# Kernel tuning notes

Hardware: AMD Instinct MI355X
Metric: run time of the kernel (lower is better)

The kernel has to match this reference:

```python
import jax, jax.numpy as jnp
import numpy as np

B, T, C = 2, 2048, 1024
H = 16
HD = C // H  # 64


def setup_inputs() -> dict:
    key = jax.random.key(0)
    ks = jax.random.split(key, 6)
    s_in = 1.0 / np.sqrt(C)
    s_pr = 1.0 / np.sqrt(H * HD)
    x = jax.random.normal(ks[0], (B, T, C), dtype=jnp.float32)
    Wq = jax.random.uniform(ks[1], (H, C, HD), jnp.float32, -s_in, s_in)
    Wk = jax.random.uniform(ks[2], (H, C, HD), jnp.float32, -s_in, s_in)
    Wv = jax.random.uniform(ks[3], (H, C, HD), jnp.float32, -s_in, s_in)
    Wp = jax.random.uniform(ks[4], (H * HD, C), jnp.float32, -s_pr, s_pr)
    bp = jax.random.uniform(ks[5], (C,), jnp.float32, -s_pr, s_pr)
    return {"x": x, "Wq": Wq, "Wk": Wk, "Wv": Wv, "Wp": Wp, "bp": bp}


def reference(x, Wq, Wk, Wv, Wp, bp):
    # per-head projections: [B,T,C] x [H,C,D] -> [B,H,T,D]
    q = jnp.einsum('btc,hcd->bhtd', x, Wq)
    k = jnp.einsum('btc,hcd->bhtd', x, Wk)
    v = jnp.einsum('btc,hcd->bhtd', x, Wv)
    scale = HD ** (-0.5)
    scores = jnp.einsum('bhtd,bhsd->bhts', q, k) * scale  # [B,H,T,T]
    causal = jnp.tril(jnp.ones((T, T), dtype=bool))
    scores = jnp.where(causal, scores, -jnp.inf)
    w = jax.nn.softmax(scores, axis=-1)
    out = jnp.einsum('bhts,bhsd->bhtd', w, v)  # [B,H,T,D]
    # concat heads: [B,T,H*D] (head order matches torch.cat over heads)
    out = jnp.transpose(out, (0, 2, 1, 3)).reshape(B, T, H * HD)
    return out @ Wp + bp
```

## Files before the change

### kernel.cpp

```cpp
#include <hip/hip_runtime.h>
#include <hip/hip_bf16.h>

#define B_NUM 2
#define T_SEQ 2048
#define C_DIM 1024
#define H_NUM 16
#define HD    64
#define M_TOT 4096
#define BH_N  32

typedef __attribute__((ext_vector_type(8))) short short8;
typedef __attribute__((ext_vector_type(4))) float floatx4;

__device__ __forceinline__ short f2bf(float f) {
    unsigned u = __float_as_uint(f);
    u += 0x7FFFu + ((u >> 16) & 1u);
    return (short)(u >> 16);
}

__device__ __forceinline__ unsigned pk2bf(float a, float b) {
    float2 f2; f2.x = a; f2.y = b;
    __hip_bfloat162 h = __float22bfloat162_rn(f2);
    unsigned u; __builtin_memcpy(&u, &h, 4); return u;
}

__device__ __forceinline__ void gld16(const short* g, short* l) {
    __builtin_amdgcn_global_load_lds(
        (const __attribute__((address_space(1))) void*)g,
        (__attribute__((address_space(3))) void*)l, 16, 0, 0);
}

__global__ __launch_bounds__(256) void convert_x(const float* __restrict__ x,
                                                 short* __restrict__ xb) {
    int idx = (blockIdx.x * 256 + threadIdx.x) * 8;
    float4 a = *(const float4*)(x + idx);
    float4 b = *(const float4*)(x + idx + 4);
    short8 o;
    o[0] = f2bf(a.x); o[1] = f2bf(a.y); o[2] = f2bf(a.z); o[3] = f2bf(a.w);
    o[4] = f2bf(b.x); o[5] = f2bf(b.y); o[6] = f2bf(b.z); o[7] = f2bf(b.w);
    *(short8*)(xb + idx) = o;
}

__global__ __launch_bounds__(256) void transp_w(
    const float* __restrict__ Wq, const float* __restrict__ Wk,
    const float* __restrict__ Wv, const float* __restrict__ Wp,
    short* __restrict__ wt, short* __restrict__ wpt) {
    const int ct = blockIdx.x, y = blockIdx.y;
    __shared__ short sh[64][72];
    const int tid = threadIdx.x;
    if (y < 48) {
        const int which = y >> 4, h = y & 15;
        const float* W = ((which == 0) ? Wq : (which == 1) ? Wk : Wv) + (size_t)h * C_DIM * HD;
        const int c0 = ct * 64;
        #pragma unroll
        for (int p = 0; p < 4; ++p) {
            int idx = tid + 256 * p;
            int c = idx >> 4, d4 = idx & 15;
            float4 v = *(const float4*)(W + (size_t)(c0 + c) * HD + d4 * 4);
            sh[d4 * 4 + 0][c] = f2bf(v.x);
            sh[d4 * 4 + 1][c] = f2bf(v.y);
            sh[d4 * 4 + 2][c] = f2bf(v.z);
            sh[d4 * 4 + 3][c] = f2bf(v.w);
        }
        __syncthreads();
        #pragma unroll
        for (int p = 0; p < 2; ++p) {
            int idx = tid + 256 * p;
            int d = idx >> 3, cc = idx & 7;
            short8 vv = *(const short8*)(&sh[d][cc * 8]);
            *(short8*)(wt + ((size_t)(which * 16 + h) * 64 + d) * C_DIM + c0 + cc * 8) = vv;
        }
    } else {
        const int nt = y - 48;
        #pragma unroll
        for (int p = 0; p < 4; ++p) {
            int idx = tid + 256 * p;
            int k = idx >> 4, n4 = idx & 15;
            float4 v = *(const float4*)(Wp + (size_t)(ct * 64 + k) * C_DIM + nt * 64 + n4 * 4);
            sh[n4 * 4 + 0][k] = f2bf(v.x);
            sh[n4 * 4 + 1][k] = f2bf(v.y);
            sh[n4 * 4 + 2][k] = f2bf(v.z);
            sh[n4 * 4 + 3][k] = f2bf(v.w);
        }
        __syncthreads();
        #pragma unroll
        for (int p = 0; p < 2; ++p) {
            int idx = tid + 256 * p;
            int n = idx >> 3, cc = idx & 7;
            short8 vv = *(const short8*)(&sh[n][cc * 8]);
            *(short8*)(wpt + (size_t)(nt * 64 + n) * C_DIM + ct * 64 + cc * 8) = vv;
        }
    }
}

__global__ __launch_bounds__(256) void qkv_gemm(
    const short* __restrict__ xb, const short* __restrict__ wt,
    short* __restrict__ qb, short* __restrict__ kb, short* __restrict__ vtb) {
    const int mt = blockIdx.x, ntg = blockIdx.y;
    const int m0 = mt * 128, n0 = ntg * 128;
    const int which = ntg >> 3;
    const float sc = (which == 0) ? 0.125f * 1.4426950408889634f : 1.0f;

    __shared__ short smem[17408];
    short* As = smem;
    short* Bs = smem + 8192;

    const int tid = threadIdx.x;
    const int lane = tid & 63, w = tid >> 6;
    const int wm = w & 1, wn = w >> 1;
    const int hi = lane >> 4, llo = lane & 15;
    const int lrow = lane >> 3;
    const int lswz = ((lane & 7) ^ (lrow & 7)) * 8;
    const int fc0 = (hi ^ (llo & 7)) * 8;
    const int fc1 = ((hi + 4) ^ (llo & 7)) * 8;

    floatx4 acc[4][4];
    #pragma unroll
    for (int i = 0; i < 4; ++i)
        #pragma unroll
        for (int j = 0; j < 4; ++j)
            #pragma unroll
            for (int r = 0; r < 4; ++r) acc[i][j][r] = 0.0f;

    const size_t a_base = (size_t)(m0 + w * 32 + lrow) * C_DIM + lswz;
    const size_t b_base = (size_t)(n0 + w * 32 + lrow) * C_DIM + lswz;

    for (int kt = 0; kt < C_DIM / 64; ++kt) {
        const int c0 = kt * 64;
        __syncthreads();
        #pragma unroll
        for (int p = 0; p < 4; ++p) {
            gld16(xb + a_base + (size_t)p * 8 * C_DIM + c0, &As[(w * 32 + p * 8) * 64]);
            gld16(wt + b_base + (size_t)p * 8 * C_DIM + c0, &Bs[(w * 32 + p * 8) * 64]);
        }
        __syncthreads();

        short8 af[4][2];
        #pragma unroll
        for (int mi = 0; mi < 4; ++mi) {
            const int row = wm * 64 + mi * 16 + llo;
            af[mi][0] = *(const short8*)(&As[row * 64 + fc0]);
            af[mi][1] = *(const short8*)(&As[row * 64 + fc1]);
        }
        #pragma unroll
        for (int ni = 0; ni < 4; ++ni) {
            const int row = wn * 64 + ni * 16 + llo;
            short8 b0 = *(const short8*)(&Bs[row * 64 + fc0]);
            short8 b1 = *(const short8*)(&Bs[row * 64 + fc1]);
            #pragma unroll
            for (int mi = 0; mi < 4; ++mi) {
                acc[mi][ni] = __builtin_amdgcn_mfma_f32_16x16x32_bf16(af[mi][0], b0, acc[mi][ni], 0, 0, 0);
                acc[mi][ni] = __builtin_amdgcn_mfma_f32_16x16x32_bf16(af[mi][1], b1, acc[mi][ni], 0, 0, 0);
            }
        }
    }
    __syncthreads();

    short (*R)[136] = (short(*)[136])smem;
    if (which == 2) {
        #pragma unroll
        for (int mi = 0; mi < 4; ++mi)
            #pragma unroll
            for (int ni = 0; ni < 4; ++ni)
                #pragma unroll
                for (int r = 0; r < 4; ++r)
                    R[wn * 64 + ni * 16 + llo][wm * 64 + mi * 16 + hi * 4 + r] =
                        f2bf(acc[mi][ni][r]);
        __syncthreads();
        const int b = m0 >> 11;
        #pragma unroll
        for (int p = 0; p < 8; ++p) {
            int idx = tid + 256 * p;
            int rr = idx >> 4, cc = idx & 15;
            short8 vv = *(const short8*)(&R[rr][cc * 8]);
            int n = n0 + rr;
            int h = (n >> 6) & 15, d = n & 63;
            int t = (m0 & 2047) + cc * 8;
            *(short8*)(vtb + ((size_t)((b * H_NUM + h) * HD + d)) * T_SEQ + t) = vv;
        }
    } else {
        short* outp = (which == 0) ? qb : kb;
        #pragma unroll
        for (int mi = 0; mi < 4; ++mi)
            #pragma unroll
            for (int ni = 0; ni < 4; ++ni)
                #pragma unroll
                for (int r = 0; r < 4; ++r)
                    R[wm * 64 + mi * 16 + hi * 4 + r][wn * 64 + ni * 16 + llo] =
                        f2bf(acc[mi][ni][r] * sc);
        __syncthreads();
        #pragma unroll
        for (int p = 0; p < 8; ++p) {
            int idx = tid + 256 * p;
            int r = idx >> 4, cc = idx & 15;
            short8 vv = *(const short8*)(&R[r][cc * 8]);
            int mg = m0 + r;
            int b = mg >> 11, t = mg & 2047;
            int n = n0 + cc * 8;
            int h = (n >> 6) & 15, d = n & 63;
            *(short8*)(outp + ((size_t)(b * H_NUM + h) * T_SEQ + t) * HD + d) = vv;
        }
    }
}

__global__ __launch_bounds__(256) void attn_mfma(
    const short* __restrict__ qb, const short* __restrict__ kb,
    const short* __restrict__ vtb, short* __restrict__ attb) {
    const int bh = blockIdx.x;
    const int y = blockIdx.y;
    const int qt = (y < 8) ? (15 - y) : (y - 8);
    const int b = bh >> 4, h = bh & 15;
    const short* K  = kb  + (size_t)bh * T_SEQ * HD;
    const short* Vt = vtb + (size_t)bh * HD * T_SEQ;

    __shared__ short Ks[2][4096];
    __shared__ short Vs[2][4096];
    __shared__ short Ones[16 * 64];
    __shared__ short Ps[128][76];

    const int tid = threadIdx.x;
    const int lane = tid & 63, w = tid >> 6;
    const int hi = lane >> 4, llo = lane & 15;
    const int lrow = lane >> 3;
    const int lswz = ((lane & 7) ^ (lrow & 7)) * 8;
    const int fc0 = (hi ^ (llo & 7)) * 8;
    const int fc1 = ((hi + 4) ^ (llo & 7)) * 8;
    const int kmax = 2 * qt + 1;

    short8 qf[2][2];
    const int qrow0 = qt * 128 + w * 32;
    #pragma unroll
    for (int g = 0; g < 2; ++g)
        #pragma unroll
        for (int kh = 0; kh < 2; ++kh)
            qf[g][kh] = *(const short8*)(qb +
                ((size_t)bh * T_SEQ + qrow0 + g * 16 + llo) * HD + kh * 32 + hi * 8);

    for (int i = tid; i < 16 * 64; i += 256)
        Ones[i] = (i < 64) ? (short)0x3F80 : (short)0;

    #pragma unroll
    for (int p = 0; p < 2; ++p) {
        gld16(K + (size_t)(w * 16 + p * 8 + lrow) * HD + lswz,
              &Ks[0][(w * 16 + p * 8) * 64]);
        gld16(Vt + (size_t)(w * 16 + p * 8 + lrow) * T_SEQ + lswz,
              &Vs[0][(w * 16 + p * 8) * 64]);
    }

    floatx4 Oa[2][5];
    #pragma unroll
    for (int g = 0; g < 2; ++g)
        #pragma unroll
        for (int n = 0; n < 5; ++n)
            #pragma unroll
            for (int r = 0; r < 4; ++r) Oa[g][n][r] = 0.0f;

    for (int kt = 0; kt <= kmax; ++kt) {
        __syncthreads();
        const int buf = kt & 1;

        if (kt + 1 <= kmax) {
            const int s0 = (kt + 1) * 64;
            const int nb = buf ^ 1;
            #pragma unroll
            for (int p = 0; p < 2; ++p) {
                gld16(K + ((size_t)s0 + w * 16 + p * 8 + lrow) * HD + lswz,
                      &Ks[nb][(w * 16 + p * 8) * 64]);
                gld16(Vt + (size_t)(w * 16 + p * 8 + lrow) * T_SEQ + s0 + lswz,
                      &Vs[nb][(w * 16 + p * 8) * 64]);
            }
        }

        short8 ak[4][2];
        #pragma unroll
        for (int nt = 0; nt < 4; ++nt) {
            const int row = nt * 16 + llo;
            ak[nt][0] = *(const short8*)(&Ks[buf][row * 64 + fc0]);
            ak[nt][1] = *(const short8*)(&Ks[buf][row * 64 + fc1]);
        }
        floatx4 sf[2][4];
        #pragma unroll
        for (int g = 0; g < 2; ++g)
            #pragma unroll
            for (int nt = 0; nt < 4; ++nt)
                #pragma unroll
                for (int r = 0; r < 4; ++r) sf[g][nt][r] = 0.0f;
        #pragma unroll
        for (int nt = 0; nt < 4; ++nt)
            #pragma unroll
            for (int kh = 0; kh < 2; ++kh)
                #pragma unroll
                for (int g = 0; g < 2; ++g)
                    sf[g][nt] = __builtin_amdgcn_mfma_f32_16x16x32_bf16(
                        ak[nt][kh], qf[g][kh], sf[g][nt], 0, 0, 0);

        const int sbase = kt * 64;
        #pragma unroll
        for (int g = 0; g < 2; ++g) {
            const int qg = qt * 128 + w * 32 + g * 16;
            if (sbase + 63 > qg) {
                const int qlane = qg + llo;
                #pragma unroll
                for (int nt = 0; nt < 4; ++nt)
                    #pragma unroll
                    for (int r = 0; r < 4; ++r)
                        if (sbase + nt * 16 + hi * 4 + r > qlane) sf[g][nt][r] = -3.0e38f;
            }
        }

        #pragma unroll
        for (int g = 0; g < 2; ++g)
            #pragma unroll
            for (int nt = 0; nt < 4; ++nt) {
                float p0 = __builtin_amdgcn_exp2f(sf[g][nt][0]);
                float p1 = __builtin_amdgcn_exp2f(sf[g][nt][1]);
                float p2 = __builtin_amdgcn_exp2f(sf[g][nt][2]);
                float p3 = __builtin_amdgcn_exp2f(sf[g][nt][3]);
                uint2 u; u.x = pk2bf(p0, p1); u.y = pk2bf(p2, p3);
                *(uint2*)(&Ps[w * 32 + g * 16 + llo][nt * 16 + hi * 4]) = u;
            }

        short8 av[5][2];
        #pragma unroll
        for (int nt2 = 0; nt2 < 4; ++nt2) {
            const int row = nt2 * 16 + llo;
            av[nt2][0] = *(const short8*)(&Vs[buf][row * 64 + fc0]);
            av[nt2][1] = *(const short8*)(&Vs[buf][row * 64 + fc1]);
        }
        av[4][0] = *(const short8*)(&Ones[llo * 64 + fc0]);
        av[4][1] = *(const short8*)(&Ones[llo * 64 + fc1]);
        short8 bp[2][2];
        #pragma unroll
        for (int g = 0; g < 2; ++g)
            #pragma unroll
            for (int kh = 0; kh < 2; ++kh)
                bp[g][kh] = *(const short8*)(&Ps[w * 32 + g * 16 + llo][kh * 32 + hi * 8]);
        #pragma unroll
        for (int nt2 = 0; nt2 < 5; ++nt2)
            #pragma unroll
            for (int kh = 0; kh < 2; ++kh)
                #pragma unroll
                for (int g = 0; g < 2; ++g)
                    Oa[g][nt2] = __builtin_amdgcn_mfma_f32_16x16x32_bf16(
                        av[nt2][kh], bp[g][kh], Oa[g][nt2], 0, 0, 0);
    }

    #pragma unroll
    for (int g = 0; g < 2; ++g) {
        float lb = __shfl(Oa[g][4][0], llo);
        float inv = 1.0f / lb;
        #pragma unroll
        for (int nt2 = 0; nt2 < 4; ++nt2) {
            uint2 u;
            u.x = pk2bf(Oa[g][nt2][0] * inv, Oa[g][nt2][1] * inv);
            u.y = pk2bf(Oa[g][nt2][2] * inv, Oa[g][nt2][3] * inv);
            *(uint2*)(&Ps[w * 32 + g * 16 + llo][nt2 * 16 + hi * 4]) = u;
        }
    }
    __syncthreads();
    #pragma unroll
    for (int p = 0; p < 4; ++p) {
        int idx = tid + 256 * p;
        int r = idx >> 3, cc = idx & 7;
        short8 vv = *(const short8*)(&Ps[r][cc * 8]);
        *(short8*)(attb + ((size_t)(b * T_SEQ + qt * 128 + r)) * C_DIM + h * HD + cc * 8) = vv;
    }
}

__global__ __launch_bounds__(256) void proj_gemm(
    const short* __restrict__ attb, const short* __restrict__ wpt,
    const float* __restrict__ bp, float* __restrict__ out) {
    const int mt = blockIdx.x, nt_g = blockIdx.y;
    const int m0 = mt * 128, n0 = nt_g * 64;

    __shared__ short As[8192];
    __shared__ short Bs[4096];

    const int tid = threadIdx.x;
    const int lane = tid & 63, w = tid >> 6;
    const int hi = lane >> 4, llo = lane & 15;
    const int lrow = lane >> 3;
    const int lswz = ((lane & 7) ^ (lrow & 7)) * 8;
    const int fc0 = (hi ^ (llo & 7)) * 8;
    const int fc1 = ((hi + 4) ^ (llo & 7)) * 8;

    floatx4 acc[2][4];
    #pragma unroll
    for (int i = 0; i < 2; ++i)
        #pragma unroll
        for (int j = 0; j < 4; ++j)
            #pragma unroll
            for (int r = 0; r < 4; ++r) acc[i][j][r] = 0.0f;

    const size_t a_base = (size_t)(m0 + w * 32 + lrow) * C_DIM + lswz;
    const size_t b_base = (size_t)(n0 + w * 16 + lrow) * C_DIM + lswz;

    for (int kt = 0; kt < C_DIM / 64; ++kt) {
        const int c0 = kt * 64;
        __syncthreads();
        #pragma unroll
        for (int p = 0; p < 4; ++p)
            gld16(attb + a_base + (size_t)p * 8 * C_DIM + c0, &As[(w * 32 + p * 8) * 64]);
        #pragma unroll
        for (int p = 0; p < 2; ++p)
            gld16(wpt + b_base + (size_t)p * 8 * C_DIM + c0, &Bs[(w * 16 + p * 8) * 64]);
        __syncthreads();

        short8 af[2][2];
        #pragma unroll
        for (int m2 = 0; m2 < 2; ++m2) {
            const int row = w * 32 + m2 * 16 + llo;
            af[m2][0] = *(const short8*)(&As[row * 64 + fc0]);
            af[m2][1] = *(const short8*)(&As[row * 64 + fc1]);
        }
        #pragma unroll
        for (int nt = 0; nt < 4; ++nt) {
            const int row = nt * 16 + llo;
            short8 b0 = *(const short8*)(&Bs[row * 64 + fc0]);
            short8 b1 = *(const short8*)(&Bs[row * 64 + fc1]);
            #pragma unroll
            for (int m2 = 0; m2 < 2; ++m2) {
                acc[m2][nt] = __builtin_amdgcn_mfma_f32_16x16x32_bf16(af[m2][0], b0, acc[m2][nt], 0, 0, 0);
                acc[m2][nt] = __builtin_amdgcn_mfma_f32_16x16x32_bf16(af[m2][1], b1, acc[m2][nt], 0, 0, 0);
            }
        }
    }

    #pragma unroll
    for (int nt = 0; nt < 4; ++nt) {
        const int n = n0 + nt * 16 + llo;
        const float bias = bp[n];
        #pragma unroll
        for (int m2 = 0; m2 < 2; ++m2)
            #pragma unroll
            for (int r = 0; r < 4; ++r) {
                int m = m0 + w * 32 + m2 * 16 + hi * 4 + r;
                out[(size_t)m * C_DIM + n] = acc[m2][nt][r] + bias;
            }
    }
}

extern "C" void kernel_launch(void* const* d_in, const int* in_sizes, int n_in,
                              void* d_out, int out_size, void* d_ws, size_t ws_size,
                              hipStream_t stream) {
    const float* x  = (const float*)d_in[0];
    const float* Wq = (const float*)d_in[1];
    const float* Wk = (const float*)d_in[2];
    const float* Wv = (const float*)d_in[3];
    const float* Wp = (const float*)d_in[4];
    const float* bp = (const float*)d_in[5];
    float* out = (float*)d_out;

    short* xb   = (short*)d_ws;
    short* wt   = xb  + (size_t)M_TOT * C_DIM;
    short* wpt  = wt  + (size_t)3 * H_NUM * HD * C_DIM;
    short* qb   = wpt + (size_t)C_DIM * C_DIM;
    short* kb   = qb  + (size_t)M_TOT * C_DIM;
    short* vtb  = kb  + (size_t)M_TOT * C_DIM;
    short* attb = vtb + (size_t)M_TOT * C_DIM;

    convert_x<<<dim3(M_TOT * C_DIM / 2048), 256, 0, stream>>>(x, xb);
    transp_w <<<dim3(16, 64), 256, 0, stream>>>(Wq, Wk, Wv, Wp, wt, wpt);
    qkv_gemm <<<dim3(M_TOT / 128, 3 * C_DIM / 128), 256, 0, stream>>>(xb, wt, qb, kb, vtb);
    attn_mfma<<<dim3(BH_N, T_SEQ / 128), 256, 0, stream>>>(qb, kb, vtb, attb);
    proj_gemm<<<dim3(M_TOT / 128, C_DIM / 64), 256, 0, stream>>>(attb, wpt, bp, out);
}
```

Before: 190.7 us.

## Merge prep kernels and split attention tile across eight waves

Fuses the x conversion and weight transpose kernels into one prep launch, removing a launch. Reworks attention to use 512 threads per block, with each wave handling 16 query rows instead of 32. This halves per-wave register state and roughly halves per-iteration MFMA work per wave, aiming for more parallel waves and better latency hiding. In exchange the K/V tile loads are spread across more waves, and the cost of the per-iteration barrier is shared among more waves.

Measured after the change: 179.4 us. 5.9% less time.

```diff
diff --git a/kernel.cpp b/kernel.cpp
--- a/kernel.cpp
+++ b/kernel.cpp
@@ -30,24 +30,26 @@
         (__attribute__((address_space(3))) void*)l, 16, 0, 0);
 }
 
-__global__ __launch_bounds__(256) void convert_x(const float* __restrict__ x,
-                                                 short* __restrict__ xb) {
-    int idx = (blockIdx.x * 256 + threadIdx.x) * 8;
-    float4 a = *(const float4*)(x + idx);
-    float4 b = *(const float4*)(x + idx + 4);
-    short8 o;
-    o[0] = f2bf(a.x); o[1] = f2bf(a.y); o[2] = f2bf(a.z); o[3] = f2bf(a.w);
-    o[4] = f2bf(b.x); o[5] = f2bf(b.y); o[6] = f2bf(b.z); o[7] = f2bf(b.w);
-    *(short8*)(xb + idx) = o;
-}
-
-__global__ __launch_bounds__(256) void transp_w(
-    const float* __restrict__ Wq, const float* __restrict__ Wk,
-    const float* __restrict__ Wv, const float* __restrict__ Wp,
-    short* __restrict__ wt, short* __restrict__ wpt) {
-    const int ct = blockIdx.x, y = blockIdx.y;
+__global__ __launch_bounds__(256) void prep(
+    const float* __restrict__ x, const float* __restrict__ Wq,
+    const float* __restrict__ Wk, const float* __restrict__ Wv,
+    const float* __restrict__ Wp,
+    short* __restrict__ xb, short* __restrict__ wt, short* __restrict__ wpt) {
+    const int bid = blockIdx.x;
+    const int tid = threadIdx.x;
+    if (bid < 2048) {
+        int idx = (bid * 256 + tid) * 8;
+        float4 a = *(const float4*)(x + idx);
+        float4 b = *(const float4*)(x + idx + 4);
+        short8 o;
+        o[0] = f2bf(a.x); o[1] = f2bf(a.y); o[2] = f2bf(a.z); o[3] = f2bf(a.w);
+        o[4] = f2bf(b.x); o[5] = f2bf(b.y); o[6] = f2bf(b.z); o[7] = f2bf(b.w);
+        *(short8*)(xb + idx) = o;
+        return;
+    }
+    const int b2 = bid - 2048;
+    const int ct = b2 & 15, y = b2 >> 4;
     __shared__ short sh[64][72];
-    const int tid = threadIdx.x;
     if (y < 48) {
         const int which = y >> 4, h = y & 15;
         const float* W = ((which == 0) ? Wq : (which == 1) ? Wk : Wv) + (size_t)h * C_DIM * HD;
@@ -203,7 +205,7 @@
     }
 }
 
-__global__ __launch_bounds__(256) void attn_mfma(
+__global__ __launch_bounds__(512) void attn_mfma(
     const short* __restrict__ qb, const short* __restrict__ kb,
     const short* __restrict__ vtb, short* __restrict__ attb) {
     const int bh = blockIdx.x;
@@ -227,33 +229,24 @@
     const int fc1 = ((hi + 4) ^ (llo & 7)) * 8;
     const int kmax = 2 * qt + 1;
 
-    short8 qf[2][2];
-    const int qrow0 = qt * 128 + w * 32;
-    #pragma unroll
-    for (int g = 0; g < 2; ++g)
-        #pragma unroll
-        for (int kh = 0; kh < 2; ++kh)
-            qf[g][kh] = *(const short8*)(qb +
-                ((size_t)bh * T_SEQ + qrow0 + g * 16 + llo) * HD + kh * 32 + hi * 8);
-
-    for (int i = tid; i < 16 * 64; i += 256)
+    short8 qf[2];
+    const int qcol0 = qt * 128 + w * 16;
+    #pragma unroll
+    for (int kh = 0; kh < 2; ++kh)
+        qf[kh] = *(const short8*)(qb +
+            ((size_t)bh * T_SEQ + qcol0 + llo) * HD + kh * 32 + hi * 8);
+
+    for (int i = tid; i < 16 * 64; i += 512)
         Ones[i] = (i < 64) ? (short)0x3F80 : (short)0;
 
-    #pragma unroll
-    for (int p = 0; p < 2; ++p) {
-        gld16(K + (size_t)(w * 16 + p * 8 + lrow) * HD + lswz,
-              &Ks[0][(w * 16 + p * 8) * 64]);
-        gld16(Vt + (size_t)(w * 16 + p * 8 + lrow) * T_SEQ + lswz,
-              &Vs[0][(w * 16 + p * 8) * 64]);
-    }
-
-    floatx4 Oa[2][5];
-    #pragma unroll
-    for (int g = 0; g < 2; ++g)
-        #pragma unroll
-        for (int n = 0; n < 5; ++n)
-            #pragma unroll
-            for (int r = 0; r < 4; ++r) Oa[g][n][r] = 0.0f;
+    gld16(K + (size_t)(w * 8 + lrow) * HD + lswz, &Ks[0][(w * 8) * 64]);
+    gld16(Vt + (size_t)(w * 8 + lrow) * T_SEQ + lswz, &Vs[0][(w * 8) * 64]);
+
+    floatx4 Oa[5];
+    #pragma unroll
+    for (int n = 0; n < 5; ++n)
+        #pragma unroll
+        for (int r = 0; r < 4; ++r) Oa[n][r] = 0.0f;
 
     for (int kt = 0; kt <= kmax; ++kt) {
         __syncthreads();
@@ -262,13 +255,8 @@
         if (kt + 1 <= kmax) {
             const int s0 = (kt + 1) * 64;
             const int nb = buf ^ 1;
-            #pragma unroll
-            for (int p = 0; p < 2; ++p) {
-                gld16(K + ((size_t)s0 + w * 16 + p * 8 + lrow) * HD + lswz,
-                      &Ks[nb][(w * 16 + p * 8) * 64]);
-                gld16(Vt + (size_t)(w * 16 + p * 8 + lrow) * T_SEQ + s0 + lswz,
-                      &Vs[nb][(w * 16 + p * 8) * 64]);
-            }
+            gld16(K + ((size_t)s0 + w * 8 + lrow) * HD + lswz, &Ks[nb][(w * 8) * 64]);
+            gld16(Vt + (size_t)(w * 8 + lrow) * T_SEQ + s0 + lswz, &Vs[nb][(w * 8) * 64]);
         }
 
         short8 ak[4][2];
@@ -278,47 +266,37 @@
             ak[nt][0] = *(const short8*)(&Ks[buf][row * 64 + fc0]);
             ak[nt][1] = *(const short8*)(&Ks[buf][row * 64 + fc1]);
         }
-        floatx4 sf[2][4];
-        #pragma unroll
-        for (int g = 0; g < 2; ++g)
+        floatx4 sf[4];
+        #pragma unroll
+        for (int nt = 0; nt < 4; ++nt)
+            #pragma unroll
+            for (int r = 0; r < 4; ++r) sf[nt][r] = 0.0f;
+        #pragma unroll
+        for (int nt = 0; nt < 4; ++nt)
+            #pragma unroll
+            for (int kh = 0; kh < 2; ++kh)
+                sf[nt] = __builtin_amdgcn_mfma_f32_16x16x32_bf16(
+                    ak[nt][kh], qf[kh], sf[nt], 0, 0, 0);
+
+        const int sbase = kt * 64;
+        if (sbase + 63 > qcol0) {
+            const int qlane = qcol0 + llo;
             #pragma unroll
             for (int nt = 0; nt < 4; ++nt)
                 #pragma unroll
-                for (int r = 0; r < 4; ++r) sf[g][nt][r] = 0.0f;
-        #pragma unroll
-        for (int nt = 0; nt < 4; ++nt)
-            #pragma unroll
-            for (int kh = 0; kh < 2; ++kh)
-                #pragma unroll
-                for (int g = 0; g < 2; ++g)
-                    sf[g][nt] = __builtin_amdgcn_mfma_f32_16x16x32_bf16(
-                        ak[nt][kh], qf[g][kh], sf[g][nt], 0, 0, 0);
-
-        const int sbase = kt * 64;
-        #pragma unroll
-        for (int g = 0; g < 2; ++g) {
-            const int qg = qt * 128 + w * 32 + g * 16;
-            if (sbase + 63 > qg) {
-                const int qlane = qg + llo;
-                #pragma unroll
-                for (int nt = 0; nt < 4; ++nt)
-                    #pragma unroll
-                    for (int r = 0; r < 4; ++r)
-                        if (sbase + nt * 16 + hi * 4 + r > qlane) sf[g][nt][r] = -3.0e38f;
-            }
-        }
-
-        #pragma unroll
-        for (int g = 0; g < 2; ++g)
-            #pragma unroll
-            for (int nt = 0; nt < 4; ++nt) {
-                float p0 = __builtin_amdgcn_exp2f(sf[g][nt][0]);
-                float p1 = __builtin_amdgcn_exp2f(sf[g][nt][1]);
-                float p2 = __builtin_amdgcn_exp2f(sf[g][nt][2]);
-                float p3 = __builtin_amdgcn_exp2f(sf[g][nt][3]);
-                uint2 u; u.x = pk2bf(p0, p1); u.y = pk2bf(p2, p3);
-                *(uint2*)(&Ps[w * 32 + g * 16 + llo][nt * 16 + hi * 4]) = u;
-            }
+                for (int r = 0; r < 4; ++r)
+                    if (sbase + nt * 16 + hi * 4 + r > qlane) sf[nt][r] = -3.0e38f;
+        }
+
+        #pragma unroll
+        for (int nt = 0; nt < 4; ++nt) {
+            float p0 = __builtin_amdgcn_exp2f(sf[nt][0]);
+            float p1 = __builtin_amdgcn_exp2f(sf[nt][1]);
+            float p2 = __builtin_amdgcn_exp2f(sf[nt][2]);
+            float p3 = __builtin_amdgcn_exp2f(sf[nt][3]);
+            uint2 u; u.x = pk2bf(p0, p1); u.y = pk2bf(p2, p3);
+            *(uint2*)(&Ps[w * 16 + llo][nt * 16 + hi * 4]) = u;
+        }
 
         short8 av[5][2];
         #pragma unroll
@@ -329,38 +307,33 @@
         }
         av[4][0] = *(const short8*)(&Ones[llo * 64 + fc0]);
         av[4][1] = *(const short8*)(&Ones[llo * 64 + fc1]);
-        short8 bp[2][2];
-        #pragma unroll
-        for (int g = 0; g < 2; ++g)
+        short8 bp[2];
+        #pragma unroll
+        for (int kh = 0; kh < 2; ++kh)
+            bp[kh] = *(const short8*)(&Ps[w * 16 + llo][kh * 32 + hi * 8]);
+        #pragma unroll
+        for (int nt2 = 0; nt2 < 5; ++nt2)
             #pragma unroll
             for (int kh = 0; kh < 2; ++kh)
-                bp[g][kh] = *(const short8*)(&Ps[w * 32 + g * 16 + llo][kh * 32 + hi * 8]);
-        #pragma unroll
-        for (int nt2 = 0; nt2 < 5; ++nt2)
-            #pragma unroll
-            for (int kh = 0; kh < 2; ++kh)
-                #pragma unroll
-                for (int g = 0; g < 2; ++g)
-                    Oa[g][nt2] = __builtin_amdgcn_mfma_f32_16x16x32_bf16(
-                        av[nt2][kh], bp[g][kh], Oa[g][nt2], 0, 0, 0);
-    }
-
-    #pragma unroll
-    for (int g = 0; g < 2; ++g) {
-        float lb = __shfl(Oa[g][4][0], llo);
+                Oa[nt2] = __builtin_amdgcn_mfma_f32_16x16x32_bf16(
+                    av[nt2][kh], bp[kh], Oa[nt2], 0, 0, 0);
+    }
+
+    {
+        float lb = __shfl(Oa[4][0], llo);
         float inv = 1.0f / lb;
         #pragma unroll
         for (int nt2 = 0; nt2 < 4; ++nt2) {
             uint2 u;
-            u.x = pk2bf(Oa[g][nt2][0] * inv, Oa[g][nt2][1] * inv);
-            u.y = pk2bf(Oa[g][nt2][2] * inv, Oa[g][nt2][3] * inv);
-            *(uint2*)(&Ps[w * 32 + g * 16 + llo][nt2 * 16 + hi * 4]) = u;
+            u.x = pk2bf(Oa[nt2][0] * inv, Oa[nt2][1] * inv);
+            u.y = pk2bf(Oa[nt2][2] * inv, Oa[nt2][3] * inv);
+            *(uint2*)(&Ps[w * 16 + llo][nt2 * 16 + hi * 4]) = u;
         }
     }
     __syncthreads();
     #pragma unroll
-    for (int p = 0; p < 4; ++p) {
-        int idx = tid + 256 * p;
+    for (int p = 0; p < 2; ++p) {
+        int idx = tid + 512 * p;
         int r = idx >> 3, cc = idx & 7;
         short8 vv = *(const short8*)(&Ps[r][cc * 8]);
         *(short8*)(attb + ((size_t)(b * T_SEQ + qt * 128 + r)) * C_DIM + h * HD + cc * 8) = vv;
@@ -459,9 +432,8 @@
     short* vtb  = kb  + (size_t)M_TOT * C_DIM;
     short* attb = vtb + (size_t)M_TOT * C_DIM;
 
-    convert_x<<<dim3(M_TOT * C_DIM / 2048), 256, 0, stream>>>(x, xb);
-    transp_w <<<dim3(16, 64), 256, 0, stream>>>(Wq, Wk, Wv, Wp, wt, wpt);
+    prep     <<<dim3(3072), 256, 0, stream>>>(x, Wq, Wk, Wv, Wp, xb, wt, wpt);
     qkv_gemm <<<dim3(M_TOT / 128, 3 * C_DIM / 128), 256, 0, stream>>>(xb, wt, qb, kb, vtb);
-    attn_mfma<<<dim3(BH_N, T_SEQ / 128), 256, 0, stream>>>(qb, kb, vtb, attb);
+    attn_mfma<<<dim3(BH_N, T_SEQ / 128), 512, 0, stream>>>(qb, kb, vtb, attb);
     proj_gemm<<<dim3(M_TOT / 128, C_DIM / 64), 256, 0, stream>>>(attb, wpt, bp, out);
 }
```
